# Performance work log

Measured on AMD Instinct MI355X. Metric: run time of the kernel, lower is better.

## Reference

```python
import jax, jax.numpy as jnp
import numpy as np

# HGT meta: 2 node types (A=0, B=1), 3 relations (src_type, dst_type)
L, T, R = 3, 2, 3
H, D = 1, 64            # PyG HGTConv default heads=1, head_dim = hidden/heads
F = H * D               # hidden_channels = input feature dim = 64
NA = NB = 131072
E = 1_000_000
REL = [(0, 1), (1, 0), (0, 0)]


def setup_inputs() -> dict:
    key = jax.random.key(0)
    ks = jax.random.split(key, 16)
    sc = 1.0 / np.sqrt(F)
    inp = {}
    inp["xA"] = jax.random.normal(ks[0], (NA, F), jnp.float32)
    inp["xB"] = jax.random.normal(ks[1], (NB, F), jnp.float32)
    # K/Q/V projections per (layer, node_type)
    inp["Wk"] = jax.random.normal(ks[2], (L, T, F, F), jnp.float32) * sc
    inp["bk"] = jnp.zeros((L, T, F), jnp.float32)
    inp["Wq"] = jax.random.normal(ks[3], (L, T, F, F), jnp.float32) * sc
    inp["bq"] = jnp.zeros((L, T, F), jnp.float32)
    inp["Wv"] = jax.random.normal(ks[4], (L, T, F, F), jnp.float32) * sc
    inp["bv"] = jnp.zeros((L, T, F), jnp.float32)
    # per (layer, relation, head) attention / message matrices and priority
    inp["a_rel"] = jax.random.normal(ks[5], (L, R, H, D, D), jnp.float32) * sc
    inp["m_rel"] = jax.random.normal(ks[6], (L, R, H, D, D), jnp.float32) * sc
    inp["p_rel"] = jnp.ones((L, R, H), jnp.float32)
    # output projection + skip gate per (layer, node_type)
    inp["Wa"] = jax.random.normal(ks[7], (L, T, F, F), jnp.float32) * sc
    inp["ba"] = jnp.zeros((L, T, F), jnp.float32)
    inp["skip"] = jnp.ones((L, T), jnp.float32)
    # final readout Linear(hidden, 1)
    inp["lin_w"] = jax.random.normal(ks[8], (F, 1), jnp.float32) * sc
    inp["lin_b"] = jnp.zeros((1,), jnp.float32)
    # edge indices: ei[0]=src, ei[1]=dst (NA == NB so one range works)
    inp["ei1"] = jax.random.randint(ks[9], (2, E), 0, NA, jnp.int32)   # A -> B
    inp["ei2"] = jax.random.randint(ks[10], (2, E), 0, NA, jnp.int32)  # B -> A
    inp["ei3"] = jax.random.randint(ks[11], (2, E), 0, NA, jnp.int32)  # A -> A
    return inp


def _hgt_layer(xs, eis, Wk, bk, Wq, bq, Wv, bv, a_rel, m_rel, p_rel, Wa, ba, skip):
    # per-type K/Q/V projections, reshaped to [N, H, D]
    k = [(xs[t] @ Wk[t] + bk[t]).reshape(-1, H, D) for t in range(T)]
    q = [(xs[t] @ Wq[t] + bq[t]).reshape(-1, H, D) for t in range(T)]
    v = [(xs[t] @ Wv[t] + bv[t]).reshape(-1, H, D) for t in range(T)]
    agg = [jnp.zeros((xs[t].shape[0], H, D), xs[t].dtype) for t in range(T)]
    inv_sqrt_d = jnp.asarray(1.0 / np.sqrt(D), xs[0].dtype)
    for r, (s, d) in enumerate(REL):
        src, dst = eis[r][0], eis[r][1]
        n_d = xs[d].shape[0]
        # relation-specific transforms on source nodes, then edge gather
        k_r = jnp.einsum('nhd,hde->nhe', k[s], a_rel[r])
        v_r = jnp.einsum('nhd,hde->nhe', v[s], m_rel[r])
        # attention score per edge per head: (q_dst . k_src) * p_rel / sqrt(D)
        score = jnp.einsum('ehd,ehd->eh', q[d][dst], k_r[src]) * p_rel[r] * inv_sqrt_d
        # segment softmax over incoming edges of each dst node (per edge type)
        mx = jax.ops.segment_max(score, dst, num_segments=n_d)
        ex = jnp.exp(score - mx[dst])
        den = jax.ops.segment_sum(ex, dst, num_segments=n_d)
        alpha = ex / den[dst]                      # [E, H]
        msg = alpha[:, :, None] * v_r[src]         # [E, H, D]
        agg[d] = agg[d] + jax.ops.segment_sum(msg, dst, num_segments=n_d)
    outs = []
    for t in range(T):
        o = jax.nn.gelu(agg[t].reshape(-1, F), approximate=False) @ Wa[t] + ba[t]
        a = jax.nn.sigmoid(skip[t])               # skip gate (out_dim == in_dim)
        outs.append(a * o + (1.0 - a) * xs[t])
    return outs


def reference(xA, xB, Wk, bk, Wq, bq, Wv, bv, a_rel, m_rel, p_rel, Wa, ba, skip,
              lin_w, lin_b, ei1, ei2, ei3):
    xs = [xA, xB]
    eis = [ei1, ei2, ei3]
    for l in range(L):
        xs = _hgt_layer(xs, eis, Wk[l], bk[l], Wq[l], bq[l], Wv[l], bv[l],
                        a_rel[l], m_rel[l], p_rel[l], Wa[l], ba[l], skip[l])
    x = jnp.concatenate(xs, axis=0)               # concat all node types
    pooled = jnp.sum(x, axis=0, keepdims=True)    # global_add_pool, batch=None
    return pooled @ lin_w + lin_b                 # Linear(hidden, 1) -> [1, 1]
```

## Files before the change

### kernel.cpp

```cpp
#include <hip/hip_runtime.h>
#include <cmath>

#define DEV __device__ __forceinline__

typedef __attribute__((ext_vector_type(8))) short short8v;
typedef __attribute__((ext_vector_type(4))) float f32x4;

DEV float atomicAddF(float* p, float v) {
    return unsafeAtomicAdd(p, v);
}

DEV float gelu_exact(float v) {
    return 0.5f * v * (1.f + erff(v * 0.70710678118654752f));
}

DEV unsigned short f32_to_bf16(float f) {
    union { float f; unsigned int u; } x; x.f = f;
    unsigned int r = x.u + 0x7fffu + ((x.u >> 16) & 1u);
    return (unsigned short)(r >> 16);
}

DEV unsigned int f4_to_fp8x4(float a, float b, float c, float d) {
    int r = __builtin_amdgcn_cvt_pk_fp8_f32(a, b, 0, false);
    r = __builtin_amdgcn_cvt_pk_fp8_f32(c, d, r, true);
    return (unsigned int)r;
}

DEV float4 fp8x4_to_f4(unsigned int w) {
    auto lo = __builtin_amdgcn_cvt_pk_f32_fp8(w, false);
    auto hi = __builtin_amdgcn_cvt_pk_f32_fp8(w, true);
    return make_float4(lo[0], lo[1], hi[0], hi[1]);
}

DEV short8v cvt8_bf16(float4 f0, float4 f1) {
    union { unsigned int u[4]; short8v s; } r;
    asm("v_cvt_pk_bf16_f32 %0, %1, %2" : "=v"(r.u[0]) : "v"(f0.x), "v"(f0.y));
    asm("v_cvt_pk_bf16_f32 %0, %1, %2" : "=v"(r.u[1]) : "v"(f0.z), "v"(f0.w));
    asm("v_cvt_pk_bf16_f32 %0, %1, %2" : "=v"(r.u[2]) : "v"(f1.x), "v"(f1.y));
    asm("v_cvt_pk_bf16_f32 %0, %1, %2" : "=v"(r.u[3]) : "v"(f1.z), "v"(f1.w));
    return r.s;
}


struct MatSetB {
    const unsigned short* Wt[3];
    const float* b[3];
    float*       y[3];
    int          mode[3];
    int          n;
};

#define BCAP2 6144
#define SB_TILE 4096
#define PSTR 129

__global__ __launch_bounds__(256) void combine_w_bf16(
    const float* __restrict__ Wk, const float* __restrict__ bk,
    const float* __restrict__ Wv, const float* __restrict__ bv,
    const float* __restrict__ a_rel, const float* __restrict__ m_rel,
    const float* __restrict__ p_rel, unsigned short* __restrict__ CWt,
    float* __restrict__ Cb)
{
    const int r = blockIdx.x, kv = blockIdx.y, l = blockIdx.z;
    const int srcT[3] = {0, 1, 0};
    const int s = srcT[r];
    const float* Wsrc = (kv == 0 ? Wk : Wv) + ((size_t)(l*2 + s)) * 4096;
    const float* bsrc = (kv == 0 ? bk : bv) + ((size_t)(l*2 + s)) * 64;
    const float* A    = (kv == 0 ? a_rel : m_rel) + ((size_t)(l*3 + r)) * 4096;
    const float scale = (kv == 0) ? p_rel[l*3 + r] * 0.125f : 1.f;

    __shared__ float Ws[4096];
    __shared__ float As[4096];
    const int tid = threadIdx.x;
    for (int k = tid; k < 4096; k += 256) { Ws[k] = Wsrc[k]; As[k] = A[k]; }
    __syncthreads();

    unsigned short* out = CWt + ((size_t)(l*6 + r*2 + kv)) * 4096;
    const int j = tid & 63;
    #pragma unroll
    for (int i = 0; i < 16; i++) {
        const int f = (tid >> 6) * 16 + i;
        float acc = 0.f;
        #pragma unroll
        for (int e = 0; e < 64; e++) acc = fmaf(Ws[f*64 + e], As[e*64 + j], acc);
        const int so = (l == 0) ? f : (4*(f & 15) + (f >> 4));
        out[j*64 + so] = f32_to_bf16(acc * scale);
    }
    if (tid < 64) {
        float acc = 0.f;
        for (int e = 0; e < 64; e++) acc = fmaf(bsrc[e], As[e*64 + tid], acc);
        Cb[(size_t)(l*6 + r*2 + kv) * 64 + tid] = acc * scale;
    }
}

__global__ __launch_bounds__(256) void prep_wt(
    const float* __restrict__ Wq, const float* __restrict__ Wa,
    unsigned short* __restrict__ Wqt, unsigned short* __restrict__ Wat)
{
    const int bid = blockIdx.x;
    const float* src; unsigned short* dst; int useSigma;
    if (bid < 6) { src = Wq + (size_t)bid * 4096; dst = Wqt + (size_t)bid * 4096;
                   useSigma = (bid >= 2); }
    else         { src = Wa + (size_t)(bid - 6) * 4096; dst = Wat + (size_t)(bid - 6) * 4096;
                   useSigma = 1; }
    for (int idx = threadIdx.x; idx < 4096; idx += 256) {
        const int c = idx >> 6, s = idx & 63;
        const int k = useSigma ? (16*(s & 3) + (s >> 2)) : s;
        dst[c*64 + s] = f32_to_bf16(src[k*64 + c]);
    }
}

__global__ __launch_bounds__(256) void proj_mfma(const float* __restrict__ x, MatSetB ms)
{
    const int tid = threadIdx.x;
    const int wv  = tid >> 6;
    const int ln  = tid & 63;
    const int j   = ln & 15;
    const int g   = ln >> 4;
    const long long rowb = (long long)blockIdx.x * 128 + wv * 32;

    short8v A[2][2];
    #pragma unroll
    for (int rg = 0; rg < 2; rg++) {
        const float* xp = x + (rowb + rg*16 + j) * 64 + g*8;
        #pragma unroll
        for (int ks = 0; ks < 2; ks++) {
            const float4 f0 = *(const float4*)(xp + ks*32);
            const float4 f1 = *(const float4*)(xp + ks*32 + 4);
            A[rg][ks] = cvt8_bf16(f0, f1);
        }
    }

    unsigned int kst[2][4];
    for (int m = 0; m < ms.n; m++) {
        short8v B[4][2];
        #pragma unroll
        for (int ct = 0; ct < 4; ct++) {
            const unsigned short* wp = ms.Wt[m] + (ct*16 + j) * 64 + g*8;
            B[ct][0] = *(const short8v*)(wp);
            B[ct][1] = *(const short8v*)(wp + 32);
        }
        f32x4 acc[2][4];
        #pragma unroll
        for (int ct = 0; ct < 4; ct++) {
            const float bm = ms.b[m][ct*16 + j];
            f32x4 bi = {bm, bm, bm, bm};
            acc[0][ct] = bi; acc[1][ct] = bi;
        }
        #pragma unroll
        for (int rg = 0; rg < 2; rg++)
            #pragma unroll
            for (int ct = 0; ct < 4; ct++) {
                acc[rg][ct] = __builtin_amdgcn_mfma_f32_16x16x32_bf16(
                    A[rg][0], B[ct][0], acc[rg][ct], 0, 0, 0);
                acc[rg][ct] = __builtin_amdgcn_mfma_f32_16x16x32_bf16(
                    A[rg][1], B[ct][1], acc[rg][ct], 0, 0, 0);
            }
        const int mode = ms.mode[m];
        if (mode == 0) {
            float* yb = ms.y[m];
            #pragma unroll
            for (int rg = 0; rg < 2; rg++)
                #pragma unroll
                for (int i = 0; i < 4; i++) {
                    const long long node = rowb + rg*16 + g*4 + i;
                    *(float4*)(yb + node*64 + j*4) = make_float4(
                        acc[rg][0][i], acc[rg][1][i], acc[rg][2][i], acc[rg][3][i]);
                }
        } else if (mode == 1) {
            #pragma unroll
            for (int rg = 0; rg < 2; rg++)
                #pragma unroll
                for (int i = 0; i < 4; i++)
                    kst[rg][i] = f4_to_fp8x4(
                        acc[rg][0][i], acc[rg][1][i], acc[rg][2][i], acc[rg][3][i]);
        } else {
            unsigned char* yb = (unsigned char*)ms.y[m];
            #pragma unroll
            for (int rg = 0; rg < 2; rg++)
                #pragma unroll
                for (int i = 0; i < 4; i++) {
                    const long long node = rowb + rg*16 + g*4 + i;
                    uint2 s;
                    s.x = kst[rg][i];
                    s.y = f4_to_fp8x4(
                        acc[rg][0][i], acc[rg][1][i], acc[rg][2][i], acc[rg][3][i]);
                    *(uint2*)(yb + node*128 + j*8) = s;
                }
        }
    }
}

__global__ __launch_bounds__(256) void scatter_bucket(
    const int* __restrict__ ei, int E, int nbuck,
    int* __restrict__ bcur, int2* __restrict__ pairbuf)
{
    __shared__ int  hist[256];
    __shared__ int  lbase[256];
    __shared__ int  gbase[256];
    __shared__ int  lcur[256];
    __shared__ int  scanbuf[256];
    __shared__ int2 stage[SB_TILE];
    const int tid = threadIdx.x;
    const int tile0 = blockIdx.x * SB_TILE;

    int2 my[16]; int mb[16];
    #pragma unroll
    for (int i = 0; i < 16; i++) {
        const int e = tile0 + tid + i*256;
        if (e < E) { my[i].x = ei[e]; my[i].y = ei[E + e]; mb[i] = my[i].y >> 9; }
        else mb[i] = -1;
    }
    hist[tid] = 0;
    __syncthreads();
    #pragma unroll
    for (int i = 0; i < 16; i++) if (mb[i] >= 0) atomicAdd(&hist[mb[i]], 1);
    __syncthreads();
    const int c = hist[tid];
    scanbuf[tid] = c;
    __syncthreads();
    for (int off = 1; off < 256; off <<= 1) {
        int add = (tid >= off) ? scanbuf[tid - off] : 0;
        __syncthreads();
        scanbuf[tid] += add;
        __syncthreads();
    }
    lbase[tid] = scanbuf[tid] - c;
    lcur[tid]  = scanbuf[tid] - c;
    if (c > 0 && tid < nbuck) gbase[tid] = atomicAdd(bcur + tid * 16, c);
    __syncthreads();
    #pragma unroll
    for (int i = 0; i < 16; i++) {
        if (mb[i] >= 0) {
            const int p = atomicAdd(&lcur[mb[i]], 1);
            stage[p] = my[i];
        }
    }
    __syncthreads();
    if (c > 0 && tid < nbuck) {
        const int gb = gbase[tid];
        const int lb = lbase[tid];
        int2* dstp = pairbuf + (size_t)tid * BCAP2;
        for (int jj = 0; jj < c; jj++) {
            const int gp = gb + jj;
            if (gp < BCAP2) dstp[gp] = stage[lb + jj];
        }
    }
}

__global__ __launch_bounds__(256) void bucket_csr(
    const int2* __restrict__ pairbuf, const int* __restrict__ bcur,
    int* __restrict__ row_ptr, int* __restrict__ row_end,
    int* __restrict__ col, int n)
{
    const int b   = blockIdx.x;
    const int tid = threadIdx.x;
    __shared__ int lcnt[512];
    __shared__ int lcur[512];
    __shared__ int scanbuf[256];
    int cnt = bcur[b * 16];
    if (cnt > BCAP2) cnt = BCAP2;
    lcnt[tid] = 0; lcnt[tid + 256] = 0;
    __syncthreads();
    const int2* src = pairbuf + (size_t)b * BCAP2;
    for (int i = tid; i < cnt; i += 256)
        atomicAdd(&lcnt[src[i].y & 511], 1);
    __syncthreads();
    const int c0 = lcnt[2*tid], c1 = lcnt[2*tid + 1];
    const int s = c0 + c1;
    scanbuf[tid] = s;
    __syncthreads();
    for (int off = 1; off < 256; off <<= 1) {
        int add = (tid >= off) ? scanbuf[tid - off] : 0;
        __syncthreads();
        scanbuf[tid] += add;
        __syncthreads();
    }
    const int excl = scanbuf[tid] - s;
    const int base = b * BCAP2;
    const int d0 = (b << 9) + 2*tid;
    if (d0 < n)     { row_ptr[d0]   = base + excl;      row_end[d0]   = base + excl + c0; }
    if (d0 + 1 < n) { row_ptr[d0+1] = base + excl + c0; row_end[d0+1] = base + excl + c0 + c1; }
    lcur[2*tid] = excl; lcur[2*tid + 1] = excl + c0;
    __syncthreads();
    for (int i = tid; i < cnt; i += 256) {
        const int2 p = src[i];
        const int pos = atomicAdd(&lcur[p.y & 511], 1);
        col[base + pos] = p.x;
    }
}

#define AGG_BODY(RP, RE, COL, KV, O0, O1)                                              \
    {                                                                                  \
        float4 acc0 = {0.f,0.f,0.f,0.f}, acc1 = {0.f,0.f,0.f,0.f};                     \
        float ssum = 0.f;                                                              \
        const int s0 = RP[dst], s1 = RE[dst];                                          \
        int src_cur = (s0 < s1) ? COL[s0] : 0;                                         \
        uint4 kvr = *(const uint4*)(KV + (size_t)src_cur * 128 + sub*16);              \
        for (int e = s0; e < s1; e++) {                                                \
            const int src_next = (e + 1 < s1) ? COL[e + 1] : 0;                        \
            const uint4 kvn = *(const uint4*)(KV + (size_t)src_next * 128 + sub*16);   \
            const float4 kA = fp8x4_to_f4(kvr.x);                                      \
            const float4 kB = fp8x4_to_f4(kvr.z);                                      \
            float sc = q0.x*kA.x + q0.y*kA.y + q0.z*kA.z + q0.w*kA.w                   \
                     + q1.x*kB.x + q1.y*kB.y + q1.z*kB.z + q1.w*kB.w;                  \
            sc += __shfl_xor(sc, 1); sc += __shfl_xor(sc, 2); sc += __shfl_xor(sc, 4); \
            const float p = __expf(sc);                                                \
            const float4 vA = fp8x4_to_f4(kvr.y);                                      \
            const float4 vB = fp8x4_to_f4(kvr.w);                                      \
            ssum += p;                                                                 \
            acc0.x = fmaf(p, vA.x, acc0.x); acc0.y = fmaf(p, vA.y, acc0.y);            \
            acc0.z = fmaf(p, vA.z, acc0.z); acc0.w = fmaf(p, vA.w, acc0.w);            \
            acc1.x = fmaf(p, vB.x, acc1.x); acc1.y = fmaf(p, vB.y, acc1.y);            \
            acc1.z = fmaf(p, vB.z, acc1.z); acc1.w = fmaf(p, vB.w, acc1.w);            \
            kvr = kvn;                                                                 \
        }                                                                              \
        const float inv = (ssum > 0.f) ? 1.f / ssum : 0.f;                             \
        O0.x = fmaf(acc0.x, inv, O0.x); O0.y = fmaf(acc0.y, inv, O0.y);                \
        O0.z = fmaf(acc0.z, inv, O0.z); O0.w = fmaf(acc0.w, inv, O0.w);                \
        O1.x = fmaf(acc1.x, inv, O1.x); O1.y = fmaf(acc1.y, inv, O1.y);                \
        O1.z = fmaf(acc1.z, inv, O1.z); O1.w = fmaf(acc1.w, inv, O1.w);                \
    }

__global__ __launch_bounds__(256) void agg_epilogue(
    const int* __restrict__ rp1, const int* __restrict__ re1, const int* __restrict__ c1,
    const int* __restrict__ rp2, const int* __restrict__ re2, const int* __restrict__ c2,
    const float* __restrict__ q,
    const unsigned char* __restrict__ kva, const unsigned char* __restrict__ kvb,
    float* __restrict__ xio, const unsigned short* __restrict__ Wat,
    const float* __restrict__ ba, const float* __restrict__ skipw,
    int xstd, int dual, int dopool, float* __restrict__ vec)
{
    __shared__ float lds[64 * PSTR];
    __shared__ float lds_pool[64];
    const int tid = threadIdx.x;
    const long long rowb = (long long)blockIdx.x * 128;
    if (tid < 64) lds_pool[tid] = 0.f;

    const int sub = tid & 7;
    #pragma unroll
    for (int rep = 0; rep < 4; rep++) {
        const int dl  = rep*32 + (tid >> 3);
        const int dst = (int)rowb + dl;
        const float4* qp = (const float4*)(q + (size_t)dst * 64);
        const float4 q0 = qp[sub*2], q1 = qp[sub*2 + 1];
        float4 o0 = {0.f,0.f,0.f,0.f}, o1 = {0.f,0.f,0.f,0.f};
        AGG_BODY(rp1, re1, c1, kva, o0, o1)
        if (dual) {
            AGG_BODY(rp2, re2, c2, kvb, o0, o1)
        }
        float* lp = lds + (size_t)(8*sub) * PSTR + dl;
        lp[0*PSTR] = gelu_exact(o0.x); lp[1*PSTR] = gelu_exact(o0.y);
        lp[2*PSTR] = gelu_exact(o0.z); lp[3*PSTR] = gelu_exact(o0.w);
        lp[4*PSTR] = gelu_exact(o1.x); lp[5*PSTR] = gelu_exact(o1.y);
        lp[6*PSTR] = gelu_exact(o1.z); lp[7*PSTR] = gelu_exact(o1.w);
    }
    __syncthreads();

    const int wv = tid >> 6;
    const int ln = tid & 63;
    const int j  = ln & 15;
    const int g  = ln >> 4;

    short8v A[2][2];
    #pragma unroll
    for (int rg = 0; rg < 2; rg++) {
        const int r = wv*32 + rg*16 + j;
        #pragma unroll
        for (int ks = 0; ks < 2; ks++) {
            const int pb = g*8 + ks*32;
            const float4 f0 = make_float4(lds[(pb+0)*PSTR + r], lds[(pb+1)*PSTR + r],
                                          lds[(pb+2)*PSTR + r], lds[(pb+3)*PSTR + r]);
            const float4 f1 = make_float4(lds[(pb+4)*PSTR + r], lds[(pb+5)*PSTR + r],
                                          lds[(pb+6)*PSTR + r], lds[(pb+7)*PSTR + r]);
            A[rg][ks] = cvt8_bf16(f0, f1);
        }
    }

    short8v B[4][2];
    #pragma unroll
    for (int ct = 0; ct < 4; ct++) {
        const unsigned short* wp = Wat + (ct*16 + j) * 64 + g*8;
        B[ct][0] = *(const short8v*)(wp);
        B[ct][1] = *(const short8v*)(wp + 32);
    }
    f32x4 acc[2][4];
    #pragma unroll
    for (int ct = 0; ct < 4; ct++) {
        const float bm = ba[ct*16 + j];
        f32x4 bi = {bm, bm, bm, bm};
        acc[0][ct] = bi; acc[1][ct] = bi;
    }
    #pragma unroll
    for (int rg = 0; rg < 2; rg++)
        #pragma unroll
        for (int ct = 0; ct < 4; ct++) {
            acc[rg][ct] = __builtin_amdgcn_mfma_f32_16x16x32_bf16(
                A[rg][0], B[ct][0], acc[rg][ct], 0, 0, 0);
            acc[rg][ct] = __builtin_amdgcn_mfma_f32_16x16x32_bf16(
                A[rg][1], B[ct][1], acc[rg][ct], 0, 0, 0);
        }

    const float gate = 1.f / (1.f + __expf(-skipw[0]));
    const float og   = 1.f - gate;
    float4 pacc = {0.f,0.f,0.f,0.f};
    #pragma unroll
    for (int rg = 0; rg < 2; rg++)
        #pragma unroll
        for (int i = 0; i < 4; i++) {
            const long long node = rowb + wv*32 + rg*16 + g*4 + i;
            float* xp = xio + node*64;
            float4 o;
            if (xstd) {
                o.x = gate*acc[rg][0][i] + og*xp[j];
                o.y = gate*acc[rg][1][i] + og*xp[16 + j];
                o.z = gate*acc[rg][2][i] + og*xp[32 + j];
                o.w = gate*acc[rg][3][i] + og*xp[48 + j];
            } else {
                const float4 xo = *(const float4*)(xp + 4*j);
                o = make_float4(gate*acc[rg][0][i] + og*xo.x,
                                gate*acc[rg][1][i] + og*xo.y,
                                gate*acc[rg][2][i] + og*xo.z,
                                gate*acc[rg][3][i] + og*xo.w);
            }
            if (!dopool) {
                *(float4*)(xp + 4*j) = o;
            } else {
                pacc.x += o.x; pacc.y += o.y; pacc.z += o.z; pacc.w += o.w;
            }
        }
    if (dopool) {
        atomicAdd(&lds_pool[4*j + 0], pacc.x);
        atomicAdd(&lds_pool[4*j + 1], pacc.y);
        atomicAdd(&lds_pool[4*j + 2], pacc.z);
        atomicAdd(&lds_pool[4*j + 3], pacc.w);
        __syncthreads();
        if (tid < 64) atomicAddF(vec + tid, lds_pool[tid]);
    }
}

__global__ void final_dot(const float* __restrict__ vec, const float* __restrict__ lw,
                          const float* __restrict__ lb, float* __restrict__ out)
{
    const int i = threadIdx.x;
    float v = vec[i] * lw[16*(i & 3) + (i >> 2)];
    #pragma unroll
    for (int m = 32; m >= 1; m >>= 1) v += __shfl_xor(v, m);
    if (i == 0) out[0] = v + lb[0];
}

extern "C" void kernel_launch(void* const* d_in, const int* in_sizes, int n_in,
                              void* d_out, int out_size, void* d_ws, size_t ws_size,
                              hipStream_t stream)
{
    float* xs[2] = {(float*)d_in[0], (float*)d_in[1]};
    const float* Wk    = (const float*)d_in[2];
    const float* bk    = (const float*)d_in[3];
    const float* Wq    = (const float*)d_in[4];
    const float* bq    = (const float*)d_in[5];
    const float* Wv    = (const float*)d_in[6];
    const float* bv    = (const float*)d_in[7];
    const float* a_rel = (const float*)d_in[8];
    const float* m_rel = (const float*)d_in[9];
    const float* p_rel = (const float*)d_in[10];
    const float* Wa    = (const float*)d_in[11];
    const float* ba    = (const float*)d_in[12];
    const float* skipw = (const float*)d_in[13];
    const float* lin_w = (const float*)d_in[14];
    const float* lin_b = (const float*)d_in[15];
    const int*   ei[3] = {(const int*)d_in[16], (const int*)d_in[17], (const int*)d_in[18]};

    const long long NA = in_sizes[0] / 64;
    const long long NB = in_sizes[1] / 64;
    const long long Ns[2] = {NA, NB};
    const long long Nmax = NA > NB ? NA : NB;
    int E[3];
    for (int r = 0; r < 3; r++) E[r] = in_sizes[16 + r] / 2;
    static const int dstN_is_B[3] = {1, 0, 0};
    const long long nbuckMax = (Nmax + 511) >> 9;

    float* w = (float*)d_ws;
    float* qbuf  = w; w += Nmax * 64;
    unsigned char* kv0 = (unsigned char*)w; w += Nmax * 32;
    unsigned char* kv1 = (unsigned char*)w; w += Nmax * 32;
    unsigned short* CWt = (unsigned short*)w; w += 18 * 2048;
    unsigned short* Wqt = (unsigned short*)w; w += 6 * 2048;
    unsigned short* Wat = (unsigned short*)w; w += 6 * 2048;
    float* Cb    = w; w += 18 * 64;
    float* vec   = w; w += 64;
    int* iw = (int*)w;
    int* row_ptr[3]; int* row_end[3]; int* col[3];
    for (int r = 0; r < 3; r++) {
        row_ptr[r] = iw; iw += Nmax;
        row_end[r] = iw; iw += Nmax;
        col[r]     = iw; iw += nbuckMax * BCAP2;
    }
    int*  bcur    = iw; iw += nbuckMax * 16;
    int2* pairbuf = (int2*)iw;

    combine_w_bf16<<<dim3(3, 2, 3), 256, 0, stream>>>(Wk, bk, Wv, bv, a_rel, m_rel, p_rel, CWt, Cb);
    prep_wt<<<12, 256, 0, stream>>>(Wq, Wa, Wqt, Wat);
    hipMemsetAsync(vec, 0, 64 * sizeof(float), stream);

    for (int r = 0; r < 3; r++) {
        const int n = (int)Ns[dstN_is_B[r]];
        const int nbuck = (n + 511) >> 9;
        hipMemsetAsync(bcur, 0, (size_t)nbuck * 16 * sizeof(int), stream);
        scatter_bucket<<<(E[r] + SB_TILE - 1) / SB_TILE, 256, 0, stream>>>(
            ei[r], E[r], nbuck, bcur, pairbuf);
        bucket_csr<<<nbuck, 256, 0, stream>>>(pairbuf, bcur, row_ptr[r], row_end[r], col[r], n);
    }

    const int gA = (int)(NA >> 7), gB = (int)(NB >> 7);
    for (int l = 0; l < 3; l++) {
        const int xstd   = (l == 0) ? 1 : 0;
        const int dopool = (l == 2) ? 1 : 0;
        {
            MatSetB ms; ms.n = 3;
            ms.Wt[0] = Wqt + (size_t)(l*2 + 1) * 4096;  ms.b[0] = bq + (size_t)(l*2 + 1) * 64;
            ms.y[0] = qbuf;        ms.mode[0] = 0;
            ms.Wt[1] = CWt + (size_t)(l*6 + 2) * 4096;  ms.b[1] = Cb + (size_t)(l*6 + 2) * 64;
            ms.y[1] = nullptr;     ms.mode[1] = 1;
            ms.Wt[2] = CWt + (size_t)(l*6 + 3) * 4096;  ms.b[2] = Cb + (size_t)(l*6 + 3) * 64;
            ms.y[2] = (float*)kv1; ms.mode[2] = 2;
            proj_mfma<<<gB, 256, 0, stream>>>(xs[1], ms);
        }
        {
            MatSetB ms; ms.n = 2;
            ms.Wt[0] = CWt + (size_t)(l*6 + 0) * 4096;  ms.b[0] = Cb + (size_t)(l*6 + 0) * 64;
            ms.y[0] = nullptr;     ms.mode[0] = 1;
            ms.Wt[1] = CWt + (size_t)(l*6 + 1) * 4096;  ms.b[1] = Cb + (size_t)(l*6 + 1) * 64;
            ms.y[1] = (float*)kv0; ms.mode[1] = 2;
            ms.Wt[2] = ms.Wt[1]; ms.b[2] = ms.b[1]; ms.y[2] = ms.y[1]; ms.mode[2] = 2;
            proj_mfma<<<gA, 256, 0, stream>>>(xs[0], ms);
        }
        agg_epilogue<<<gB, 256, 0, stream>>>(
            row_ptr[0], row_end[0], col[0],
            row_ptr[0], row_end[0], col[0],
            qbuf, kv0, kv0, xs[1],
            Wat + (size_t)(l*2 + 1) * 4096, ba + (size_t)(l*2 + 1) * 64,
            skipw + l*2 + 1, xstd, 0, dopool, vec);

        {
            MatSetB ms; ms.n = 3;
            ms.Wt[0] = Wqt + (size_t)(l*2 + 0) * 4096;  ms.b[0] = bq + (size_t)(l*2 + 0) * 64;
            ms.y[0] = qbuf;        ms.mode[0] = 0;
            ms.Wt[1] = CWt + (size_t)(l*6 + 4) * 4096;  ms.b[1] = Cb + (size_t)(l*6 + 4) * 64;
            ms.y[1] = nullptr;     ms.mode[1] = 1;
            ms.Wt[2] = CWt + (size_t)(l*6 + 5) * 4096;  ms.b[2] = Cb + (size_t)(l*6 + 5) * 64;
            ms.y[2] = (float*)kv0; ms.mode[2] = 2;
            proj_mfma<<<gA, 256, 0, stream>>>(xs[0], ms);
        }
        agg_epilogue<<<gA, 256, 0, stream>>>(
            row_ptr[1], row_end[1], col[1],
            row_ptr[2], row_end[2], col[2],
            qbuf, kv1, kv0, xs[0],
            Wat + (size_t)(l*2 + 0) * 4096, ba + (size_t)(l*2 + 0) * 64,
            skipw + l*2 + 0, xstd, 1, dopool, vec);
    }

    final_dot<<<1, 64, 0, stream>>>(vec, lin_w, lin_b, (float*)d_out);
}
```

Before: 857.4 us.

## Use 1024-thread blocks in agg_epilogue, one destination row per thread-group

The aggregation epilogue now launches 1024 threads per 128-row block. Each 8-thread group handles one destination row instead of looping over four rows per 256-thread block. The MFMA output projection runs on the first 8 wavefronts, each covering 16 rows, and the weight loads move into the MFMA loop. This exposes more parallel gather latency per block, at the cost of larger blocks, an idle half during the GEMM, and register pressure from launch_bounds(1024, 8).

```diff
diff --git a/kernel.cpp b/kernel.cpp
--- a/kernel.cpp
+++ b/kernel.cpp
@@ -322,7 +322,7 @@
         O1.z = fmaf(acc1.z, inv, O1.z); O1.w = fmaf(acc1.w, inv, O1.w);                \
     }
 
-__global__ __launch_bounds__(256) void agg_epilogue(
+__global__ __launch_bounds__(1024, 8) void agg_epilogue(
     const int* __restrict__ rp1, const int* __restrict__ re1, const int* __restrict__ c1,
     const int* __restrict__ rp2, const int* __restrict__ re2, const int* __restrict__ c2,
     const float* __restrict__ q,
@@ -337,10 +337,9 @@
     const long long rowb = (long long)blockIdx.x * 128;
     if (tid < 64) lds_pool[tid] = 0.f;
 
-    const int sub = tid & 7;
-    #pragma unroll
-    for (int rep = 0; rep < 4; rep++) {
-        const int dl  = rep*32 + (tid >> 3);
+    {
+        const int sub = tid & 7;
+        const int dl  = tid >> 3;
         const int dst = (int)rowb + dl;
         const float4* qp = (const float4*)(q + (size_t)dst * 64);
         const float4 q0 = qp[sub*2], q1 = qp[sub*2 + 1];
@@ -357,15 +356,14 @@
     }
     __syncthreads();
 
-    const int wv = tid >> 6;
-    const int ln = tid & 63;
-    const int j  = ln & 15;
-    const int g  = ln >> 4;
-
-    short8v A[2][2];
-    #pragma unroll
-    for (int rg = 0; rg < 2; rg++) {
-        const int r = wv*32 + rg*16 + j;
+    if (tid < 512) {
+        const int wv = tid >> 6;
+        const int ln = tid & 63;
+        const int j  = ln & 15;
+        const int g  = ln >> 4;
+        const int r  = wv*16 + j;
+
+        short8v A[2];
         #pragma unroll
         for (int ks = 0; ks < 2; ks++) {
             const int pb = g*8 + ks*32;
@@ -373,55 +371,43 @@
                                           lds[(pb+2)*PSTR + r], lds[(pb+3)*PSTR + r]);
             const float4 f1 = make_float4(lds[(pb+4)*PSTR + r], lds[(pb+5)*PSTR + r],
                                           lds[(pb+6)*PSTR + r], lds[(pb+7)*PSTR + r]);
-            A[rg][ks] = cvt8_bf16(f0, f1);
-        }
-    }
-
-    short8v B[4][2];
-    #pragma unroll
-    for (int ct = 0; ct < 4; ct++) {
-        const unsigned short* wp = Wat + (ct*16 + j) * 64 + g*8;
-        B[ct][0] = *(const short8v*)(wp);
-        B[ct][1] = *(const short8v*)(wp + 32);
-    }
-    f32x4 acc[2][4];
-    #pragma unroll
-    for (int ct = 0; ct < 4; ct++) {
-        const float bm = ba[ct*16 + j];
-        f32x4 bi = {bm, bm, bm, bm};
-        acc[0][ct] = bi; acc[1][ct] = bi;
-    }
-    #pragma unroll
-    for (int rg = 0; rg < 2; rg++)
+            A[ks] = cvt8_bf16(f0, f1);
+        }
+
+        f32x4 acc[4];
         #pragma unroll
         for (int ct = 0; ct < 4; ct++) {
-            acc[rg][ct] = __builtin_amdgcn_mfma_f32_16x16x32_bf16(
-                A[rg][0], B[ct][0], acc[rg][ct], 0, 0, 0);
-            acc[rg][ct] = __builtin_amdgcn_mfma_f32_16x16x32_bf16(
-                A[rg][1], B[ct][1], acc[rg][ct], 0, 0, 0);
-        }
-
-    const float gate = 1.f / (1.f + __expf(-skipw[0]));
-    const float og   = 1.f - gate;
-    float4 pacc = {0.f,0.f,0.f,0.f};
-    #pragma unroll
-    for (int rg = 0; rg < 2; rg++)
+            const float bm = ba[ct*16 + j];
+            acc[ct] = (f32x4){bm, bm, bm, bm};
+        }
+        #pragma unroll
+        for (int ct = 0; ct < 4; ct++) {
+            const unsigned short* wp = Wat + (ct*16 + j) * 64 + g*8;
+            const short8v B0 = *(const short8v*)(wp);
+            const short8v B1 = *(const short8v*)(wp + 32);
+            acc[ct] = __builtin_amdgcn_mfma_f32_16x16x32_bf16(A[0], B0, acc[ct], 0, 0, 0);
+            acc[ct] = __builtin_amdgcn_mfma_f32_16x16x32_bf16(A[1], B1, acc[ct], 0, 0, 0);
+        }
+
+        const float gate = 1.f / (1.f + __expf(-skipw[0]));
+        const float og   = 1.f - gate;
+        float4 pacc = {0.f,0.f,0.f,0.f};
         #pragma unroll
         for (int i = 0; i < 4; i++) {
-            const long long node = rowb + wv*32 + rg*16 + g*4 + i;
+            const long long node = rowb + wv*16 + g*4 + i;
             float* xp = xio + node*64;
             float4 o;
             if (xstd) {
-                o.x = gate*acc[rg][0][i] + og*xp[j];
-                o.y = gate*acc[rg][1][i] + og*xp[16 + j];
-                o.z = gate*acc[rg][2][i] + og*xp[32 + j];
-                o.w = gate*acc[rg][3][i] + og*xp[48 + j];
+                o.x = gate*acc[0][i] + og*xp[j];
+                o.y = gate*acc[1][i] + og*xp[16 + j];
+                o.z = gate*acc[2][i] + og*xp[32 + j];
+                o.w = gate*acc[3][i] + og*xp[48 + j];
             } else {
                 const float4 xo = *(const float4*)(xp + 4*j);
-                o = make_float4(gate*acc[rg][0][i] + og*xo.x,
-                                gate*acc[rg][1][i] + og*xo.y,
-                                gate*acc[rg][2][i] + og*xo.z,
-                                gate*acc[rg][3][i] + og*xo.w);
+                o = make_float4(gate*acc[0][i] + og*xo.x,
+                                gate*acc[1][i] + og*xo.y,
+                                gate*acc[2][i] + og*xo.z,
+                                gate*acc[3][i] + og*xo.w);
             }
             if (!dopool) {
                 *(float4*)(xp + 4*j) = o;
@@ -429,14 +415,15 @@
                 pacc.x += o.x; pacc.y += o.y; pacc.z += o.z; pacc.w += o.w;
             }
         }
-    if (dopool) {
-        atomicAdd(&lds_pool[4*j + 0], pacc.x);
-        atomicAdd(&lds_pool[4*j + 1], pacc.y);
-        atomicAdd(&lds_pool[4*j + 2], pacc.z);
-        atomicAdd(&lds_pool[4*j + 3], pacc.w);
-        __syncthreads();
-        if (tid < 64) atomicAddF(vec + tid, lds_pool[tid]);
-    }
+        if (dopool) {
+            atomicAdd(&lds_pool[4*j + 0], pacc.x);
+            atomicAdd(&lds_pool[4*j + 1], pacc.y);
+            atomicAdd(&lds_pool[4*j + 2], pacc.z);
+            atomicAdd(&lds_pool[4*j + 3], pacc.w);
+        }
+    }
+    __syncthreads();
+    if (dopool && tid < 64) atomicAddF(vec + tid, lds_pool[tid]);
 }
 
 __global__ void final_dot(const float* __restrict__ vec, const float* __restrict__ lw,
@@ -534,7 +521,7 @@
             ms.Wt[2] = ms.Wt[1]; ms.b[2] = ms.b[1]; ms.y[2] = ms.y[1]; ms.mode[2] = 2;
             proj_mfma<<<gA, 256, 0, stream>>>(xs[0], ms);
         }
-        agg_epilogue<<<gB, 256, 0, stream>>>(
+        agg_epilogue<<<gB, 1024, 0, stream>>>(
             row_ptr[0], row_end[0], col[0],
             row_ptr[0], row_end[0], col[0],
             qbuf, kv0, kv0, xs[1],
@@ -551,7 +538,7 @@
             ms.y[2] = (float*)kv0; ms.mode[2] = 2;
             proj_mfma<<<gA, 256, 0, stream>>>(xs[0], ms);
         }
-        agg_epilogue<<<gA, 256, 0, stream>>>(
+        agg_epilogue<<<gA, 1024, 0, stream>>>(
             row_ptr[1], row_end[1], col[1],
             row_ptr[2], row_end[2], col[2],
             qbuf, kv1, kv0, xs[0],
```

Result: faster. 823.0 us (-4.0%).
